# Kernel optimization log

Measured on AMD Instinct MI355X. Metric: run time of the kernel, lower is better.

The kernel has to match this reference:

```python
import jax, jax.numpy as jnp
import numpy as np

N = 50000      # nodes
E = 800000     # edges (avg degree 16)
IN = 128       # in_channels
OUT = 128      # out_channels
H1, C1 = 4, 64 # conv1: 4 heads x 64 -> concat 256
H2, C2 = 1, OUT
NEG_SLOPE = 0.2


def setup_inputs() -> dict:
    key = jax.random.key(0)
    ks = jax.random.split(key, 10)
    def glorot(k, shape, fan):
        return jax.random.normal(k, shape, jnp.float32) * (1.0 / np.sqrt(fan))
    x = jax.random.normal(ks[0], (N, IN), jnp.float32)
    edge_index = jax.random.randint(ks[1], (2, E), 0, N)
    W1 = glorot(ks[2], (IN, H1 * C1), IN)
    att_src1 = glorot(ks[3], (H1, C1), C1)
    att_dst1 = glorot(ks[4], (H1, C1), C1)
    b1 = jnp.zeros((H1 * C1,), jnp.float32)
    W2 = glorot(ks[5], (H1 * C1, H2 * C2), H1 * C1)
    att_src2 = glorot(ks[6], (H2, C2), C2)
    att_dst2 = glorot(ks[7], (H2, C2), C2)
    b2 = jnp.zeros((OUT,), jnp.float32)
    return {"x": x, "edge_index": edge_index,
            "W1": W1, "att_src1": att_src1, "att_dst1": att_dst1, "b1": b1,
            "W2": W2, "att_src2": att_src2, "att_dst2": att_dst2, "b2": b2}


def gat_conv(x, src, dst, W, att_s, att_d, bias, heads, ch):
    """PyG GATConv: linear -> edge attention -> per-dst softmax -> scatter-sum."""
    n = x.shape[0]
    h = (x @ W).reshape(n, heads, ch)                      # [N, H, C]
    a_s = jnp.einsum('nhc,hc->nh', h, att_s)               # [N, H]
    a_d = jnp.einsum('nhc,hc->nh', h, att_d)               # [N, H]
    e = jax.nn.leaky_relu(a_s[src] + a_d[dst], NEG_SLOPE)  # [Etot, H]
    e_max = jax.ops.segment_max(e, dst, num_segments=n)    # [N, H]
    e = jnp.exp(e - e_max[dst])
    denom = jax.ops.segment_sum(e, dst, num_segments=n)    # [N, H]
    alpha = e / (denom[dst] + 1e-16)                        # [Etot, H]
    msg = h[src] * alpha[:, :, None]                        # [Etot, H, C]
    out = jax.ops.segment_sum(msg, dst, num_segments=n)     # [N, H, C]
    return out.reshape(n, heads * ch) + bias


def reference(x, edge_index, W1, att_src1, att_dst1, b1, W2, att_src2, att_dst2, b2):
    n = x.shape[0]
    loop = jnp.arange(n)
    # GATConv(add_self_loops=True): append (i, i) edges
    src = jnp.concatenate([edge_index[0], loop])
    dst = jnp.concatenate([edge_index[1], loop])
    h = jax.nn.relu(gat_conv(x, src, dst, W1, att_src1, att_dst1, b1, H1, C1))
    out = jax.nn.relu(gat_conv(h, src, dst, W2, att_src2, att_dst2, b2, H2, C2))
    return out
```

## Files before the change

### kernel.cpp

```cpp
#include <hip/hip_runtime.h>
#include <hip/hip_bf16.h>
#include <hip/hip_fp16.h>


#define NEG_SLOPE 0.2f

typedef __attribute__((ext_vector_type(8))) _Float16 f16x8;
typedef __attribute__((ext_vector_type(8))) short s16x8;
typedef __attribute__((ext_vector_type(4))) float f32x4;

__device__ inline void loadH8(float* v, const __half* p) {
    union { s16x8 raw; __half2 h2[4]; } u;
    u.raw = *(const s16x8*)p;
#pragma unroll
    for (int i = 0; i < 4; ++i) {
        float2 f = __half22float2(u.h2[i]);
        v[2 * i] = f.x;
        v[2 * i + 1] = f.y;
    }
}

__device__ inline f16x8 loadAfrag(const __half* __restrict__ p) {
    return *(const f16x8*)p;
}
__device__ inline f16x8 loadAfrag(const float* __restrict__ p) {
    float4 a = *(const float4*)p;
    float4 b = *(const float4*)(p + 4);
    union { f16x8 v; __half hv[8]; } u;
    u.hv[0] = __float2half(a.x); u.hv[1] = __float2half(a.y);
    u.hv[2] = __float2half(a.z); u.hv[3] = __float2half(a.w);
    u.hv[4] = __float2half(b.x); u.hv[5] = __float2half(b.y);
    u.hv[6] = __float2half(b.z); u.hv[7] = __float2half(b.w);
    return u.v;
}


__device__ inline void pack_w_elem(const float* __restrict__ W, __half* __restrict__ bp,
                                   int K, int N, int tid) {
    int k = tid / N, n = tid - k * N;
    int ks = k >> 5, k5 = k & 31, quad = k5 >> 3, j = k5 & 7;
    int ct = n >> 4;
    int lane = quad * 16 + (n & 15);
    size_t idx = ((size_t)(ct * (K >> 5) + ks) * 64 + lane) * 8 + j;
    bp[idx] = __float2half(W[tid]);
}

__global__ __launch_bounds__(256) void pack_prep(
        const float* __restrict__ W1, __half* __restrict__ bp1,
        const float* __restrict__ W2, __half* __restrict__ bp2,
        int* __restrict__ zp, int zn) {
    int tid = blockIdx.x * blockDim.x + threadIdx.x;
    if (tid < 128 * 256) pack_w_elem(W1, bp1, 128, 256, tid);
    if (tid < 256 * 128) pack_w_elem(W2, bp2, 256, 128, tid);
    for (int i = tid; i < zn; i += 32768) zp[i] = 0;
}


template<int K, int NN, int H, bool ATOMIC, typename AT>
__device__ void gemm_body(int bx, int M,
        const AT* __restrict__ A, const __half* __restrict__ Bp,
        const float* __restrict__ att_s, const float* __restrict__ att_d,
        float* __restrict__ as_, float* __restrict__ ad_,
        __half* __restrict__ Hout) {
    constexpr int KS = K >> 5;
    constexpr int CW = NN / 64;
    constexpr int RW = 4 / CW;
    constexpr int C = NN / H;
    const int lane = threadIdx.x & 63;
    const int w = threadIdx.x >> 6;
    const int wr = w / CW;
    const int wc = w % CW;
    const int quad = lane >> 4;
    const int r16 = lane & 15;
    const int mBase = bx * (RW * 32) + wr * 32;
    const int nBase = wc * 64;
    const int head = nBase / C;

    f32x4 acc[2][4];
#pragma unroll
    for (int rt = 0; rt < 2; ++rt)
#pragma unroll
        for (int ct = 0; ct < 4; ++ct) acc[rt][ct] = (f32x4){0.f, 0.f, 0.f, 0.f};

#pragma unroll
    for (int ks = 0; ks < KS; ++ks) {
        f16x8 af[2];
#pragma unroll
        for (int rt = 0; rt < 2; ++rt) {
            int row = mBase + rt * 16 + r16;
            if (row < M) {
                af[rt] = loadAfrag(A + (size_t)row * K + ks * 32 + quad * 8);
            } else {
                af[rt] = (f16x8){0, 0, 0, 0, 0, 0, 0, 0};
            }
        }
        f16x8 bf[4];
#pragma unroll
        for (int ct = 0; ct < 4; ++ct) {
            int ctg = (nBase >> 4) + ct;
            size_t off = ((size_t)(ctg * KS + ks) * 64 + lane) * 8;
            bf[ct] = *(const f16x8*)(Bp + off);
        }
#pragma unroll
        for (int rt = 0; rt < 2; ++rt)
#pragma unroll
            for (int ct = 0; ct < 4; ++ct)
                acc[rt][ct] = __builtin_amdgcn_mfma_f32_16x16x32_f16(af[rt], bf[ct], acc[rt][ct], 0, 0, 0);
    }

#pragma unroll
    for (int rt = 0; rt < 2; ++rt)
#pragma unroll
        for (int ct = 0; ct < 4; ++ct) {
            int row0 = mBase + rt * 16 + quad * 4;
            int col = nBase + ct * 16 + r16;
#pragma unroll
            for (int r = 0; r < 4; ++r) {
                int row = row0 + r;
                if (row < M) Hout[(size_t)row * NN + col] = __float2half(acc[rt][ct][r]);
            }
        }

    float attS[4], attD[4];
#pragma unroll
    for (int ct = 0; ct < 4; ++ct) {
        int cc = (nBase % C) + ct * 16 + r16;
        attS[ct] = att_s[head * C + cc];
        attD[ct] = att_d[head * C + cc];
    }
#pragma unroll
    for (int rt = 0; rt < 2; ++rt)
#pragma unroll
        for (int r = 0; r < 4; ++r) {
            float ps = 0.f, pd = 0.f;
#pragma unroll
            for (int ct = 0; ct < 4; ++ct) {
                ps += acc[rt][ct][r] * attS[ct];
                pd += acc[rt][ct][r] * attD[ct];
            }
#pragma unroll
            for (int off = 1; off < 16; off <<= 1) {
                ps += __shfl_xor(ps, off);
                pd += __shfl_xor(pd, off);
            }
            int row = mBase + rt * 16 + quad * 4 + r;
            if (r16 == 0 && row < M) {
                if (ATOMIC) {
                    atomicAdd(&as_[row * H + head], ps);
                    atomicAdd(&ad_[row * H + head], pd);
                } else {
                    as_[row * H + head] = ps;
                    ad_[row * H + head] = pd;
                }
            }
        }
}


__global__ __launch_bounds__(256) void gemm1_scatter(
        int EPB, const int* __restrict__ ei, int E, int N,
        int* __restrict__ cnt, int* __restrict__ csr_src,
        const float* __restrict__ x, const __half* __restrict__ Bp,
        const float* __restrict__ att_s, const float* __restrict__ att_d,
        float* __restrict__ as_, float* __restrict__ ad_,
        __half* __restrict__ Hout) {
    const int Etot = E + N;
    int e0 = blockIdx.x * EPB;
    int e1 = e0 + EPB; if (e1 > Etot) e1 = Etot;
    for (int e = e0 + (int)threadIdx.x; e < e1; e += 256) {
        int s, d;
        if (e < E) { s = ei[e]; d = ei[E + e]; } else { s = e - E; d = s; }
        int r = atomicAdd(&cnt[d], 1);
        if (r < 64) csr_src[(d << 6) + r] = s;
    }
    gemm_body<128, 256, 4, false, float>(blockIdx.x, N, x, Bp,
                                         att_s, att_d, as_, ad_, Hout);
}

__global__ __launch_bounds__(256) void gemm2_kernel(
        int M, const __half* __restrict__ A, const __half* __restrict__ Bp,
        const float* __restrict__ att_s, const float* __restrict__ att_d,
        float* __restrict__ as_, float* __restrict__ ad_,
        __half* __restrict__ Hout) {
    gemm_body<256, 128, 1, true, __half>(blockIdx.x, M, A, Bp,
                                         att_s, att_d, as_, ad_, Hout);
}


__device__ inline float edge_w(float a) {
    float e = a > 0.f ? a : NEG_SLOPE * a;
    return __expf(e);
}

template<int U, int HC, int H, int GRP>
__device__ inline void agg_step(int p, const int* __restrict__ csr_src,
                                const __half* __restrict__ h,
                                const float* __restrict__ as_, float adv,
                                int c0, int head, float* acc, float& den) {
    int srcv[U];
#pragma unroll
    for (int u = 0; u < U; ++u) srcv[u] = csr_src[p + u * GRP];
    float f[U][8];
#pragma unroll
    for (int u = 0; u < U; ++u) loadH8(f[u], h + (size_t)srcv[u] * HC + c0);
    float wv[U];
#pragma unroll
    for (int u = 0; u < U; ++u) wv[u] = edge_w(as_[srcv[u] * H + head] + adv);
#pragma unroll
    for (int u = 0; u < U; ++u) den += wv[u];
#pragma unroll
    for (int u = 0; u < U; ++u)
#pragma unroll
        for (int i = 0; i < 8; ++i) acc[i] += wv[u] * f[u][i];
}

template<int HC, int H, bool F16OUT>
__global__ __launch_bounds__(256) void fused_agg(int N,
                                                 const int* __restrict__ cnt,
                                                 const int* __restrict__ csr_src,
                                                 const __half* __restrict__ h,
                                                 const float* __restrict__ as_,
                                                 const float* __restrict__ ad_,
                                                 const float* __restrict__ bias,
                                                 float* __restrict__ out,
                                                 __half* __restrict__ outh) {
    constexpr int LPE = HC / 8;
    constexpr int GRP = 64 / LPE;
    constexpr int C = HC / H;
    const int n = blockIdx.x * 4 + (threadIdx.x >> 6);
    if (n >= N) return;
    const int lane = threadIdx.x & 63;
    const int g = lane / LPE;
    const int lq = lane % LPE;
    const int c0 = lq * 8;
    const int head = c0 / C;
    const int s0 = n << 6;
    int deg = cnt[n]; if (deg > 64) deg = 64;
    const int s1 = s0 + deg;
    const float adv = ad_[n * H + head];
    float acc[8] = {};
    float den = 0.f;
    int p = s0 + g;
    for (; p + 3 * GRP < s1; p += 4 * GRP)
        agg_step<4, HC, H, GRP>(p, csr_src, h, as_, adv, c0, head, acc, den);
    for (; p < s1; p += GRP)
        agg_step<1, HC, H, GRP>(p, csr_src, h, as_, adv, c0, head, acc, den);
#pragma unroll
    for (int off = LPE; off < 64; off <<= 1) {
        den += __shfl_xor(den, off);
#pragma unroll
        for (int i = 0; i < 8; ++i) acc[i] += __shfl_xor(acc[i], off);
    }
    if (g == 0) {
        float dinv = 1.0f / (den + 1e-16f);
        float o[8];
#pragma unroll
        for (int i = 0; i < 8; ++i) {
            float v = acc[i] * dinv + bias[c0 + i];
            o[i] = v > 0.f ? v : 0.f;
        }
        if (F16OUT) {
            union { s16x8 raw; __half hv[8]; } u;
#pragma unroll
            for (int i = 0; i < 8; ++i) u.hv[i] = __float2half(o[i]);
            *(s16x8*)(outh + (size_t)n * HC + c0) = u.raw;
        } else {
            float4 v0 = make_float4(o[0], o[1], o[2], o[3]);
            float4 v1 = make_float4(o[4], o[5], o[6], o[7]);
            *(float4*)(out + (size_t)n * HC + c0) = v0;
            *(float4*)(out + (size_t)n * HC + c0 + 4) = v1;
        }
    }
}

extern "C" void kernel_launch(void* const* d_in, const int* in_sizes, int n_in,
                              void* d_out, int out_size, void* d_ws, size_t ws_size,
                              hipStream_t stream) {
    const float* x      = (const float*)d_in[0];
    const int*   ei     = (const int*)d_in[1];
    const float* W1     = (const float*)d_in[2];
    const float* att_s1 = (const float*)d_in[3];
    const float* att_d1 = (const float*)d_in[4];
    const float* b1     = (const float*)d_in[5];
    const float* W2     = (const float*)d_in[6];
    const float* att_s2 = (const float*)d_in[7];
    const float* att_d2 = (const float*)d_in[8];
    const float* b2     = (const float*)d_in[9];
    float* out = (float*)d_out;

    const int N_ = in_sizes[0] / 128;
    const int E_ = in_sizes[1] / 2;
    const int Etot = E_ + N_;

    __half* h1 = (__half*)d_ws;
    __half* x2 = h1 + (size_t)N_ * 256;
    __half* bp1 = x2 + (size_t)N_ * 256;
    __half* bp2 = bp1 + 32768;
    float* as1 = (float*)(bp2 + 32768);
    float* ad1 = as1 + (size_t)N_ * 4;
    int*   cnt = (int*)(ad1 + (size_t)N_ * 4);
    float* as2 = (float*)(cnt + N_);
    float* ad2 = as2 + N_;
    int* csr_src = (int*)(ad2 + N_);

    int G1B = (N_ + 31) / 32;
    int G2B = (N_ + 63) / 64;
    int EPB = (Etot + G1B - 1) / G1B;

    pack_prep<<<128, 256, 0, stream>>>(W1, bp1, W2, bp2, cnt, 3 * N_);

    gemm1_scatter<<<G1B, 256, 0, stream>>>(
        EPB, ei, E_, N_, cnt, csr_src, x, bp1, att_s1, att_d1, as1, ad1, h1);
    fused_agg<256, 4, true><<<(N_ + 3) / 4, 256, 0, stream>>>(
        N_, cnt, csr_src, h1, as1, ad1, b1, nullptr, x2);

    __half* h2 = h1;
    gemm2_kernel<<<G2B, 256, 0, stream>>>(
        N_, x2, bp2, att_s2, att_d2, as2, ad2, h2);
    fused_agg<128, 1, false><<<(N_ + 3) / 4, 256, 0, stream>>>(
        N_, cnt, csr_src, h2, as2, ad2, b2, out, nullptr);

    (void)n_in; (void)out_size; (void)ws_size;
}
```

Before: 270.6 us.

## Split edge scatter into separate blocks, pad counters, prefill self-loops

The edge-to-CSR scatter moves out of the GEMM blocks into its own blocks within the same launch, one edge per thread, so the GEMM and scatter work proceed in parallel instead of serially inside each block. Per-node counters are padded to 128-byte stride to cut atomic contention and false sharing on shared cache lines. Self-loops are written in the prep kernel by initialising each count to 1 and setting slot 0 to the node itself. This grows the zeroed counter region 32x and adds more blocks to the launch.

```diff
diff --git a/kernel.cpp b/kernel.cpp
--- a/kernel.cpp
+++ b/kernel.cpp
@@ -48,11 +48,15 @@
 __global__ __launch_bounds__(256) void pack_prep(
         const float* __restrict__ W1, __half* __restrict__ bp1,
         const float* __restrict__ W2, __half* __restrict__ bp2,
-        int* __restrict__ zp, int zn) {
+        int* __restrict__ zp, int zn, int n32,
+        int* __restrict__ csr_src, int N) {
     int tid = blockIdx.x * blockDim.x + threadIdx.x;
     if (tid < 128 * 256) pack_w_elem(W1, bp1, 128, 256, tid);
     if (tid < 256 * 128) pack_w_elem(W2, bp2, 256, 128, tid);
-    for (int i = tid; i < zn; i += 32768) zp[i] = 0;
+    for (int i = tid; i < zn; i += 32768)
+        zp[i] = (i < n32 && (i & 31) == 0) ? 1 : 0;
+    for (int n = tid; n < N; n += 32768)
+        csr_src[n << 6] = n;
 }
 
 
@@ -158,23 +162,22 @@
 
 
 __global__ __launch_bounds__(256) void gemm1_scatter(
-        int EPB, const int* __restrict__ ei, int E, int N,
-        int* __restrict__ cnt, int* __restrict__ csr_src,
+        int G1B, const int* __restrict__ ei, int E, int N,
+        int* __restrict__ cntp, int* __restrict__ csr_src,
         const float* __restrict__ x, const __half* __restrict__ Bp,
         const float* __restrict__ att_s, const float* __restrict__ att_d,
         float* __restrict__ as_, float* __restrict__ ad_,
         __half* __restrict__ Hout) {
-    const int Etot = E + N;
-    int e0 = blockIdx.x * EPB;
-    int e1 = e0 + EPB; if (e1 > Etot) e1 = Etot;
-    for (int e = e0 + (int)threadIdx.x; e < e1; e += 256) {
-        int s, d;
-        if (e < E) { s = ei[e]; d = ei[E + e]; } else { s = e - E; d = s; }
-        int r = atomicAdd(&cnt[d], 1);
-        if (r < 64) csr_src[(d << 6) + r] = s;
-    }
-    gemm_body<128, 256, 4, false, float>(blockIdx.x, N, x, Bp,
-                                         att_s, att_d, as_, ad_, Hout);
+    if ((int)blockIdx.x < G1B) {
+        gemm_body<128, 256, 4, false, float>(blockIdx.x, N, x, Bp,
+                                             att_s, att_d, as_, ad_, Hout);
+        return;
+    }
+    int e = (blockIdx.x - G1B) * 256 + threadIdx.x;
+    if (e >= E) return;
+    int s = ei[e], d = ei[E + e];
+    int r = atomicAdd(&cntp[d << 5], 1);
+    if (r < 64) csr_src[(d << 6) + r] = s;
 }
 
 __global__ __launch_bounds__(256) void gemm2_kernel(
@@ -216,7 +219,7 @@
 
 template<int HC, int H, bool F16OUT>
 __global__ __launch_bounds__(256) void fused_agg(int N,
-                                                 const int* __restrict__ cnt,
+                                                 const int* __restrict__ cntp,
                                                  const int* __restrict__ csr_src,
                                                  const __half* __restrict__ h,
                                                  const float* __restrict__ as_,
@@ -235,7 +238,7 @@
     const int c0 = lq * 8;
     const int head = c0 / C;
     const int s0 = n << 6;
-    int deg = cnt[n]; if (deg > 64) deg = 64;
+    int deg = cntp[n << 5]; if (deg > 64) deg = 64;
     const int s1 = s0 + deg;
     const float adv = ad_[n * H + head];
     float acc[8] = {};
@@ -290,7 +293,6 @@
 
     const int N_ = in_sizes[0] / 128;
     const int E_ = in_sizes[1] / 2;
-    const int Etot = E_ + N_;
 
     __half* h1 = (__half*)d_ws;
     __half* x2 = h1 + (size_t)N_ * 256;
@@ -298,27 +300,30 @@
     __half* bp2 = bp1 + 32768;
     float* as1 = (float*)(bp2 + 32768);
     float* ad1 = as1 + (size_t)N_ * 4;
-    int*   cnt = (int*)(ad1 + (size_t)N_ * 4);
-    float* as2 = (float*)(cnt + N_);
-    float* ad2 = as2 + N_;
+    int*   cntp = (int*)(ad1 + (size_t)N_ * 4);
+    float* as2  = (float*)(cntp + (size_t)N_ * 32);
+    float* ad2  = as2 + N_;
+    int zn  = N_ * 32 + 2 * N_;
+    int n32 = N_ * 32;
     int* csr_src = (int*)(ad2 + N_);
 
     int G1B = (N_ + 31) / 32;
+    int SB  = (E_ + 255) / 256;
     int G2B = (N_ + 63) / 64;
-    int EPB = (Etot + G1B - 1) / G1B;
-
-    pack_prep<<<128, 256, 0, stream>>>(W1, bp1, W2, bp2, cnt, 3 * N_);
-
-    gemm1_scatter<<<G1B, 256, 0, stream>>>(
-        EPB, ei, E_, N_, cnt, csr_src, x, bp1, att_s1, att_d1, as1, ad1, h1);
+
+    pack_prep<<<128, 256, 0, stream>>>(W1, bp1, W2, bp2,
+                                       cntp, zn, n32, csr_src, N_);
+
+    gemm1_scatter<<<G1B + SB, 256, 0, stream>>>(
+        G1B, ei, E_, N_, cntp, csr_src, x, bp1, att_s1, att_d1, as1, ad1, h1);
     fused_agg<256, 4, true><<<(N_ + 3) / 4, 256, 0, stream>>>(
-        N_, cnt, csr_src, h1, as1, ad1, b1, nullptr, x2);
+        N_, cntp, csr_src, h1, as1, ad1, b1, nullptr, x2);
 
     __half* h2 = h1;
     gemm2_kernel<<<G2B, 256, 0, stream>>>(
         N_, x2, bp2, att_s2, att_d2, as2, ad2, h2);
     fused_agg<128, 1, false><<<(N_ + 3) / 4, 256, 0, stream>>>(
-        N_, cnt, csr_src, h2, as2, ad2, b2, out, nullptr);
+        N_, cntp, csr_src, h2, as2, ad2, b2, out, nullptr);
 
     (void)n_in; (void)out_size; (void)ws_size;
 }
```

Result: no change. 270.4 us, median of 2 (-0.1%).

## Fuse layer-1 aggregation with layer-2 GEMM and split scatter into separate blocks

Applied to the files above, without the earlier changes.

Adds a 1024-thread kernel that aggregates layer-1 messages for a 64-node tile into shared memory, then runs the layer-2 MFMA GEMM directly from that tile, computing attention logits with shared atomics. This removes the x2 intermediate round-trip through global memory, the separate gemm2 launch and its global atomics on as2/ad2. Self-loops are now pre-seeded in pack_prep, and edge scattering runs in extra blocks of the GEMM1 launch instead of each GEMM block scattering a chunk first. The risk is lower occupancy from large blocks and LDS use, and the aggregation is restricted to 16 waves per tile.

```diff
diff --git a/kernel.cpp b/kernel.cpp
--- a/kernel.cpp
+++ b/kernel.cpp
@@ -48,11 +48,14 @@
 __global__ __launch_bounds__(256) void pack_prep(
         const float* __restrict__ W1, __half* __restrict__ bp1,
         const float* __restrict__ W2, __half* __restrict__ bp2,
-        int* __restrict__ zp, int zn) {
+        int* __restrict__ cnt, int* __restrict__ csr_src, int N) {
     int tid = blockIdx.x * blockDim.x + threadIdx.x;
     if (tid < 128 * 256) pack_w_elem(W1, bp1, 128, 256, tid);
     if (tid < 256 * 128) pack_w_elem(W2, bp2, 256, 128, tid);
-    for (int i = tid; i < zn; i += 32768) zp[i] = 0;
+    for (int n = tid; n < N; n += 32768) {
+        cnt[n] = 1;
+        csr_src[n << 6] = n;
+    }
 }
 
 
@@ -158,32 +161,22 @@
 
 
 __global__ __launch_bounds__(256) void gemm1_scatter(
-        int EPB, const int* __restrict__ ei, int E, int N,
+        int G1B, const int* __restrict__ ei, int E, int N,
         int* __restrict__ cnt, int* __restrict__ csr_src,
         const float* __restrict__ x, const __half* __restrict__ Bp,
         const float* __restrict__ att_s, const float* __restrict__ att_d,
         float* __restrict__ as_, float* __restrict__ ad_,
         __half* __restrict__ Hout) {
-    const int Etot = E + N;
-    int e0 = blockIdx.x * EPB;
-    int e1 = e0 + EPB; if (e1 > Etot) e1 = Etot;
-    for (int e = e0 + (int)threadIdx.x; e < e1; e += 256) {
-        int s, d;
-        if (e < E) { s = ei[e]; d = ei[E + e]; } else { s = e - E; d = s; }
-        int r = atomicAdd(&cnt[d], 1);
-        if (r < 64) csr_src[(d << 6) + r] = s;
-    }
-    gemm_body<128, 256, 4, false, float>(blockIdx.x, N, x, Bp,
-                                         att_s, att_d, as_, ad_, Hout);
-}
-
-__global__ __launch_bounds__(256) void gemm2_kernel(
-        int M, const __half* __restrict__ A, const __half* __restrict__ Bp,
-        const float* __restrict__ att_s, const float* __restrict__ att_d,
-        float* __restrict__ as_, float* __restrict__ ad_,
-        __half* __restrict__ Hout) {
-    gemm_body<256, 128, 1, true, __half>(blockIdx.x, M, A, Bp,
-                                         att_s, att_d, as_, ad_, Hout);
+    if ((int)blockIdx.x < G1B) {
+        gemm_body<128, 256, 4, false, float>(blockIdx.x, N, x, Bp,
+                                             att_s, att_d, as_, ad_, Hout);
+        return;
+    }
+    int e = (blockIdx.x - G1B) * 256 + threadIdx.x;
+    if (e >= E) return;
+    int s = ei[e], d = ei[E + e];
+    int r = atomicAdd(&cnt[d], 1);
+    if (r < 64) csr_src[(d << 6) + r] = s;
 }
 
 
@@ -213,6 +206,119 @@
 #pragma unroll
         for (int i = 0; i < 8; ++i) acc[i] += wv[u] * f[u][i];
 }
+
+
+__global__ __launch_bounds__(1024) void agg1_gemm2(
+        int N, const int* __restrict__ cnt, const int* __restrict__ csr_src,
+        const __half* __restrict__ h1, const float* __restrict__ as1,
+        const float* __restrict__ ad1, const float* __restrict__ b1,
+        const __half* __restrict__ bp2, const float* __restrict__ att_s2,
+        const float* __restrict__ att_d2,
+        float* __restrict__ as2, float* __restrict__ ad2,
+        __half* __restrict__ h2) {
+    __shared__ __half x2t[64][264];
+    __shared__ float s_as[64], s_ad[64];
+    const int tile = blockIdx.x;
+    const int tid = threadIdx.x;
+    if (tid < 64) { s_as[tid] = 0.f; s_ad[tid] = 0.f; }
+    const int lane = tid & 63;
+    const int wv = tid >> 6;
+
+    {
+        const int g = lane >> 5;
+        const int lq = lane & 31;
+        const int c0 = lq * 8;
+        const int head = c0 >> 6;
+#pragma unroll
+        for (int k = 0; k < 4; ++k) {
+            const int nl = wv + 16 * k;
+            const int n = tile * 64 + nl;
+            float o[8] = {0.f, 0.f, 0.f, 0.f, 0.f, 0.f, 0.f, 0.f};
+            if (n < N) {
+                const int s0 = n << 6;
+                int deg = cnt[n]; if (deg > 64) deg = 64;
+                const int s1 = s0 + deg;
+                const float adv = ad1[n * 4 + head];
+                float acc[8] = {};
+                float den = 0.f;
+                int p = s0 + g;
+                for (; p + 6 < s1; p += 8)
+                    agg_step<4, 256, 4, 2>(p, csr_src, h1, as1, adv, c0, head, acc, den);
+                for (; p < s1; p += 2)
+                    agg_step<1, 256, 4, 2>(p, csr_src, h1, as1, adv, c0, head, acc, den);
+                den += __shfl_xor(den, 32);
+#pragma unroll
+                for (int i = 0; i < 8; ++i) acc[i] += __shfl_xor(acc[i], 32);
+                float dinv = 1.0f / (den + 1e-16f);
+#pragma unroll
+                for (int i = 0; i < 8; ++i) {
+                    float v = acc[i] * dinv + b1[c0 + i];
+                    o[i] = v > 0.f ? v : 0.f;
+                }
+            }
+            if (g == 0) {
+                union { s16x8 raw; __half hv[8]; } u;
+#pragma unroll
+                for (int i = 0; i < 8; ++i) u.hv[i] = __float2half(o[i]);
+                *(s16x8*)&x2t[nl][c0] = u.raw;
+            }
+        }
+    }
+    __syncthreads();
+
+    const int quad = lane >> 4;
+    const int r16 = lane & 15;
+    const int wr2 = wv & 3;
+    const int wc2 = wv >> 2;
+    f32x4 acc2[2];
+    acc2[0] = (f32x4){0.f, 0.f, 0.f, 0.f};
+    acc2[1] = (f32x4){0.f, 0.f, 0.f, 0.f};
+#pragma unroll
+    for (int ks = 0; ks < 8; ++ks) {
+        f16x8 af = *(const f16x8*)&x2t[wr2 * 16 + r16][ks * 32 + quad * 8];
+#pragma unroll
+        for (int ct = 0; ct < 2; ++ct) {
+            int ctg = wc2 * 2 + ct;
+            f16x8 bf = *(const f16x8*)(bp2 + ((size_t)(ctg * 8 + ks) * 64 + lane) * 8);
+            acc2[ct] = __builtin_amdgcn_mfma_f32_16x16x32_f16(af, bf, acc2[ct], 0, 0, 0);
+        }
+    }
+    float attS[2], attD[2];
+#pragma unroll
+    for (int ct = 0; ct < 2; ++ct) {
+        int col = wc2 * 32 + ct * 16 + r16;
+        attS[ct] = att_s2[col];
+        attD[ct] = att_d2[col];
+    }
+    const int row0 = wr2 * 16 + quad * 4;
+#pragma unroll
+    for (int r = 0; r < 4; ++r) {
+        int grow = tile * 64 + row0 + r;
+        if (grow < N) {
+#pragma unroll
+            for (int ct = 0; ct < 2; ++ct)
+                h2[(size_t)grow * 128 + wc2 * 32 + ct * 16 + r16] =
+                    __float2half(acc2[ct][r]);
+        }
+        float ps = acc2[0][r] * attS[0] + acc2[1][r] * attS[1];
+        float pd = acc2[0][r] * attD[0] + acc2[1][r] * attD[1];
+#pragma unroll
+        for (int off = 1; off < 16; off <<= 1) {
+            ps += __shfl_xor(ps, off);
+            pd += __shfl_xor(pd, off);
+        }
+        if (r16 == 0 && grow < N) {
+            atomicAdd(&s_as[row0 + r], ps);
+            atomicAdd(&s_ad[row0 + r], pd);
+        }
+    }
+    __syncthreads();
+    if (tid < 64) {
+        int grow = tile * 64 + tid;
+        if (grow < N) { as2[grow] = s_as[tid]; ad2[grow] = s_ad[tid]; }
+    }
+}
+
 
 template<int HC, int H, bool F16OUT>
 __global__ __launch_bounds__(256) void fused_agg(int N,
@@ -290,11 +396,10 @@
 
     const int N_ = in_sizes[0] / 128;
     const int E_ = in_sizes[1] / 2;
-    const int Etot = E_ + N_;
 
     __half* h1 = (__half*)d_ws;
-    __half* x2 = h1 + (size_t)N_ * 256;
-    __half* bp1 = x2 + (size_t)N_ * 256;
+    __half* h2 = h1 + (size_t)N_ * 256;
+    __half* bp1 = h2 + (size_t)N_ * 128;
     __half* bp2 = bp1 + 32768;
     float* as1 = (float*)(bp2 + 32768);
     float* ad1 = as1 + (size_t)N_ * 4;
@@ -304,19 +409,18 @@
     int* csr_src = (int*)(ad2 + N_);
 
     int G1B = (N_ + 31) / 32;
-    int G2B = (N_ + 63) / 64;
-    int EPB = (Etot + G1B - 1) / G1B;
-
-    pack_prep<<<128, 256, 0, stream>>>(W1, bp1, W2, bp2, cnt, 3 * N_);
-
-    gemm1_scatter<<<G1B, 256, 0, stream>>>(
-        EPB, ei, E_, N_, cnt, csr_src, x, bp1, att_s1, att_d1, as1, ad1, h1);
-    fused_agg<256, 4, true><<<(N_ + 3) / 4, 256, 0, stream>>>(
-        N_, cnt, csr_src, h1, as1, ad1, b1, nullptr, x2);
-
-    __half* h2 = h1;
-    gemm2_kernel<<<G2B, 256, 0, stream>>>(
-        N_, x2, bp2, att_s2, att_d2, as2, ad2, h2);
+    int SB  = (E_ + 255) / 256;
+    int TB  = (N_ + 63) / 64;
+
+    pack_prep<<<128, 256, 0, stream>>>(W1, bp1, W2, bp2, cnt, csr_src, N_);
+
+    gemm1_scatter<<<G1B + SB, 256, 0, stream>>>(
+        G1B, ei, E_, N_, cnt, csr_src, x, bp1, att_s1, att_d1, as1, ad1, h1);
+
+    agg1_gemm2<<<TB, 1024, 0, stream>>>(
+        N_, cnt, csr_src, h1, as1, ad1, b1,
+        bp2, att_s2, att_d2, as2, ad2, h2);
+
     fused_agg<128, 1, false><<<(N_ + 3) / 4, 256, 0, stream>>>(
         N_, cnt, csr_src, h2, as2, ad2, b2, out, nullptr);
 
```

Measured after the change: 291.1 us. 1.08x slower.
